# Kernel optimization log

Hardware: AMD Instinct MI355X
Metric: run time of the kernel (lower is better)

Reference implementation:

```python
import jax, jax.numpy as jnp
import numpy as np

N_NODES = 50000
N_EDGES = 800000
N_S = 32          # 0e channels in node feats
N_V = 16          # 1o channels in node feats
NB = 8            # radial bessel basis size
H = 64            # MLP hidden
S_OUT = N_S + N_V           # 48 scalar message channels (filtered 0e + dot path)
V_OUT = N_V + N_S + N_V     # 64 vector message channels (filtered 1o + sxY1 + vxY2)
NUM_IRREPS = S_OUT + V_OUT  # 112, gated by radial MLP
AVG_NEIGH = 16.0


def setup_inputs() -> dict:
    key = jax.random.key(0)
    ks = jax.random.split(key, 8)
    # scale so edge lengths fall mostly inside the envelope cutoff x_max=1
    vectors = jax.random.normal(ks[0], (N_EDGES, 3), jnp.float32) * 0.25
    node_s = jax.random.normal(ks[1], (N_NODES, N_S), jnp.float32)
    node_v = jax.random.normal(ks[2], (N_NODES, N_V, 3), jnp.float32)
    senders = jax.random.randint(ks[3], (N_EDGES,), 0, N_NODES)
    receivers = jax.random.randint(ks[4], (N_EDGES,), 0, N_NODES)
    W0 = jax.random.normal(ks[5], (NB, H), jnp.float32)
    W1 = jax.random.normal(ks[6], (H, H), jnp.float32)
    W2 = jax.random.normal(ks[7], (H, NUM_IRREPS), jnp.float32)
    return {"vectors": vectors, "node_s": node_s, "node_v": node_v,
            "W0": W0, "W1": W1, "W2": W2,
            "senders": senders, "receivers": receivers}


def _radial_embed(r):
    # r: [E,1] edge lengths. Bessel basis (x_max=1) * polynomial envelope, 0 at r==0.
    n = jnp.arange(1, NB + 1, dtype=r.dtype)            # [NB]
    safe_r = jnp.maximum(r, 1e-12)
    basis = jnp.sqrt(2.0) * jnp.sin(jnp.pi * n * r) / safe_r   # [E,NB]
    x = r
    env = (1.0 - 28.0 * x**6 + 48.0 * x**7 - 21.0 * x**8) * (x < 1.0)  # smooth cutoff
    return jnp.where(r == 0.0, 0.0, basis * env)        # [E,NB]


def reference(vectors, node_s, node_v, W0, W1, W2, senders, receivers):
    E = vectors.shape[0]
    r = jnp.linalg.norm(vectors, axis=-1, keepdims=True)          # [E,1]
    u = vectors / jnp.maximum(r, 1e-12)                            # unit vectors [E,3]

    # gather sender features
    s = node_s[senders]                                            # [E,N_S]
    v = node_v[senders]                                            # [E,N_V,3]

    # equivariant tensor-product paths against spherical harmonics of u
    # (filtered to target irreps 0e,1o). Y1 ~ u, Y2 ~ traceless u u^T.
    path_a = s[:, :, None] * u[:, None, :]                         # 0e x Y1 -> 1o [E,N_S,3]
    path_b = jnp.einsum('eci,ei->ec', v, u)                        # 1o x Y1 -> 0e [E,N_V]
    T = u[:, :, None] * u[:, None, :] - jnp.eye(3, dtype=u.dtype) / 3.0  # [E,3,3]
    path_c = jnp.sqrt(1.5) * jnp.einsum('eij,ecj->eci', T, v)      # 1o x Y2 -> 1o [E,N_V,3]

    msg_s = jnp.concatenate([s, path_b], axis=-1)                  # [E,S_OUT]
    msg_v = jnp.concatenate([v, path_a, path_c], axis=1)           # [E,V_OUT,3]

    # radial MLP gate (no bias, fan-in scaled, swish hidden, linear output)
    emb = _radial_embed(r)                                         # [E,NB]
    h = jax.nn.swish(emb @ W0 / jnp.sqrt(jnp.asarray(NB, emb.dtype)))
    h = jax.nn.swish(h @ W1 / jnp.sqrt(jnp.asarray(H, emb.dtype)))
    mix = h @ W2 / jnp.sqrt(jnp.asarray(H, emb.dtype))             # [E,NUM_IRREPS]

    msg_s = msg_s * mix[:, :S_OUT]
    msg_v = msg_v * mix[:, S_OUT:, None]

    # scatter-add to receivers
    n = node_s.shape[0]
    out_s = jnp.zeros((n, S_OUT), msg_s.dtype).at[receivers].add(msg_s)
    out_v = jnp.zeros((n, V_OUT, 3), msg_v.dtype).at[receivers].add(msg_v)

    inv = 1.0 / jnp.sqrt(AVG_NEIGH)
    return jnp.concatenate([out_s * inv, (out_v * inv).reshape(n, V_OUT * 3)], axis=-1)
```

## Files before the change

kernel.cpp:

```cpp
#include <hip/hip_runtime.h>
#include <hip/hip_fp16.h>

#define N_S 32
#define N_V 16
#define NB 8
#define HH 64
#define NIR 112
#define ROW 240
#define MROW 120
#define GCAP 64

typedef _Float16 half8 __attribute__((ext_vector_type(8)));
typedef float f32x4 __attribute__((ext_vector_type(4)));

__device__ __forceinline__ float swishf(float x) {
  return x / (1.f + __expf(-x));
}

struct ChanDesc { int path, off, mixI, i; };

__device__ __forceinline__ void mkDesc(int t, ChanDesc& d) {
  if (t < 32) { d.path = 0; d.off = t; d.mixI = t; d.i = 0; }
  else if (t < 48) { d.path = 1; d.off = 3 * (t - 32); d.mixI = t; d.i = 0; }
  else if (t < ROW) {
    int q = t - 48, c = q / 3, i = q - 3 * c;
    d.mixI = 48 + c;
    if (c < 16) { d.path = 2; d.off = q; d.i = 0; }
    else if (c < 48) { d.path = 3; d.off = c - 16; d.i = i; }
    else { d.path = 4; d.off = 3 * (c - 48); d.i = i; }
  } else { d.path = -1; d.off = 0; d.mixI = 0; d.i = 0; }
}

__device__ __forceinline__ float evalChan(const ChanDesc& d,
                                          const float* __restrict__ srow,
                                          const float* __restrict__ vrow,
                                          float mix, float u0, float u1, float u2) {
  if (d.path < 0) return 0.f;
  if (d.path == 0) return srow[d.off] * mix;
  if (d.path == 2) return vrow[d.off] * mix;
  float uo = d.i == 0 ? u0 : (d.i == 1 ? u1 : u2);
  if (d.path == 3) return srow[d.off] * uo * mix;
  float dd = vrow[d.off] * u0 + vrow[d.off + 1] * u1 + vrow[d.off + 2] * u2;
  if (d.path == 1) return dd * mix;
  return 1.22474487139f * (uo * dd - vrow[d.off + d.i] * 0.33333333333f) * mix;
}

__device__ __forceinline__ float evalChan16(const ChanDesc& d,
                                            const _Float16* __restrict__ srow,
                                            const _Float16* __restrict__ vrow,
                                            float mix, float u0, float u1, float u2) {
  if (d.path == 0) return (float)srow[d.off] * mix;
  if (d.path == 2) return (float)vrow[d.off] * mix;
  float uo = d.i == 0 ? u0 : (d.i == 1 ? u1 : u2);
  if (d.path == 3) return (float)srow[d.off] * uo * mix;
  float dd = (float)vrow[d.off] * u0 + (float)vrow[d.off + 1] * u1 + (float)vrow[d.off + 2] * u2;
  if (d.path == 1) return dd * mix;
  return 1.22474487139f * (uo * dd - (float)vrow[d.off + d.i] * 0.33333333333f) * mix;
}

__device__ __forceinline__ void radialEmb(float x, float y, float z, bool valid,
                                          float* emb, float* u0, float* u1, float* u2) {
  float r2 = x * x + y * y + z * z;
  float r = sqrtf(r2);
  float invr = 1.f / fmaxf(r, 1e-12f);
  *u0 = x * invr; *u1 = y * invr; *u2 = z * invr;
  float env = 0.f;
  if (r < 1.f) {
    float r3 = r * r2;
    float r6 = r3 * r3;
    env = 1.f + r6 * (-28.f + (48.f - 21.f * r) * r);
  }
  float coef = 1.41421356237f * invr * env;
  if (!valid || r == 0.f) coef = 0.f;
  float ph = 3.14159265358979323846f * r;
  float s1 = __sinf(ph), c1 = __cosf(ph);
  float twc = 2.f * c1;
  float sp = 0.f, sc = s1;
#pragma unroll
  for (int n = 0; n < NB; ++n) {
    emb[n] = coef * sc;
    float sn = twc * sc - sp;
    sp = sc;
    sc = sn;
  }
}


__global__ __launch_bounds__(256) void hist_kernel(const int* __restrict__ rcv,
                                                   int* __restrict__ hist, int E) {
  int e = blockIdx.x * 256 + threadIdx.x;
  if (e < E) atomicAdd(&hist[rcv[e]], 1);
}

__global__ __launch_bounds__(256) void scan1_kernel(const int* __restrict__ hist,
                                                    int* __restrict__ scanTmp,
                                                    int* __restrict__ bsum, int N) {
  __shared__ int sh[256];
  int t = threadIdx.x;
  int i = blockIdx.x * 256 + t;
  sh[t] = (i < N) ? hist[i] : 0;
  __syncthreads();
#pragma unroll
  for (int off = 1; off < 256; off <<= 1) {
    int x = (t >= off) ? sh[t - off] : 0;
    __syncthreads();
    sh[t] += x;
    __syncthreads();
  }
  if (i < N) scanTmp[i] = sh[t];
  if (t == 255) bsum[blockIdx.x] = sh[255];
}

__global__ __launch_bounds__(256) void scan2_kernel(int* __restrict__ bsum, int nb) {
  __shared__ int sh[256];
  int t = threadIdx.x;
  sh[t] = (t < nb) ? bsum[t] : 0;
  __syncthreads();
#pragma unroll
  for (int off = 1; off < 256; off <<= 1) {
    int x = (t >= off) ? sh[t - off] : 0;
    __syncthreads();
    sh[t] += x;
    __syncthreads();
  }
  int excl = (t == 0) ? 0 : sh[t - 1];
  if (t < nb) bsum[t] = excl;
}

__global__ __launch_bounds__(256) void scan3_kernel(const int* __restrict__ scanTmp,
                                                    const int* __restrict__ bsum,
                                                    const int* __restrict__ hist,
                                                    int* __restrict__ offs,
                                                    int* __restrict__ cursor, int N) {
  int i = blockIdx.x * 256 + threadIdx.x;
  if (i < N) {
    int incl = scanTmp[i] + bsum[blockIdx.x];
    offs[i + 1] = incl;
    cursor[i] = incl - hist[i];
    if (i == 0) offs[0] = 0;
  }
}

__global__ __launch_bounds__(256) void reorder_kernel(const int* __restrict__ rcv,
                                                      int* __restrict__ cursor,
                                                      int* __restrict__ sortedE, int E) {
  int e = blockIdx.x * 256 + threadIdx.x;
  if (e < E) {
    int pos = atomicAdd(&cursor[rcv[e]], 1);
    sortedE[pos] = e;
  }
}

__global__ __launch_bounds__(256) void reorderInv_kernel(const int* __restrict__ rcv,
                                                         int* __restrict__ cursor,
                                                         int* __restrict__ invPos, int E) {
  int e = blockIdx.x * 256 + threadIdx.x;
  if (e < E) {
    int pos = atomicAdd(&cursor[rcv[e]], 1);
    invPos[e] = pos;
  }
}


__global__ __launch_bounds__(256) void wconv2_kernel(const float* __restrict__ W1,
                                                     const float* __restrict__ W2,
                                                     _Float16* __restrict__ W1T,
                                                     _Float16* __restrict__ W2T) {
  int i = blockIdx.x * 256 + threadIdx.x;
  if (i < 4096) {
    int k = i >> 6, n = i & 63;
    W1T[n * 64 + k] = (_Float16)(W1[k * 64 + n] * 0.125f);
  } else if (i < 4096 + 7168) {
    int j = i - 4096;
    int k = j / 112, n = j - k * 112;
    W2T[n * 64 + k] = (_Float16)(W2[k * 112 + n] * 0.125f);
  }
}

__global__ __launch_bounds__(256) void nodeconv_kernel(const float* __restrict__ ns,
                                                       const float* __restrict__ nv,
                                                       _Float16* __restrict__ s16,
                                                       _Float16* __restrict__ v16, int N) {
  int i = blockIdx.x * 256 + threadIdx.x;
  int ts = N * N_S;
  int tv = N * N_V * 3;
  if (i < ts) s16[i] = (_Float16)ns[i];
  else if (i < ts + tv) v16[i - ts] = (_Float16)nv[i - ts];
}


__global__ __launch_bounds__(256, 4) void mlp_mfma_sorted_kernel(
    const float* __restrict__ vec,
    const float* __restrict__ W0,
    const _Float16* __restrict__ W1T,
    const _Float16* __restrict__ W2T,
    const int* __restrict__ senders,
    const int* __restrict__ invPos,
    _Float16* __restrict__ mixS,
    int E) {
  __shared__ __align__(16) _Float16 hbuf[4 * 64 * 72];
  const int lane = threadIdx.x & 63;
  const int wave = threadIdx.x >> 6;
  const int gbase = blockIdx.x * 256 + wave * 64;
  _Float16* hb = hbuf + wave * (64 * 72);

  const int m15 = lane & 15;
  const int q = lane >> 4;

  {
    int e = gbase + lane;
    bool valid = e < E;
    float x = 0.f, y = 0.f, z = 0.f;
    int snd = 0;
    if (valid) {
      const float* vp = vec + 3 * (size_t)e;
      x = vp[0]; y = vp[1]; z = vp[2];
      snd = senders[e];
    }
    float emb[NB], u0, u1, u2;
    radialEmb(x, y, z, valid, emb, &u0, &u1, &u2);
    for (int kg = 0; kg < 8; ++kg) {
      half8 pk;
#pragma unroll
      for (int kk = 0; kk < 8; ++kk) {
        int k = kg * 8 + kk;
        float a = 0.f;
#pragma unroll
        for (int n = 0; n < NB; ++n) a = fmaf(emb[n], W0[n * HH + k], a);
        pk[kk] = (_Float16)swishf(a * 0.35355339059f);
      }
      *(half8*)(hb + lane * 72 + kg * 8) = pk;
    }
    float* auxp = (float*)(hb + lane * 72 + 64);
    auxp[0] = u0; auxp[1] = u1; auxp[2] = u2;
    ((int*)auxp)[3] = snd;
  }

  half8 bW1[4][2];
#pragma unroll
  for (int nt = 0; nt < 4; ++nt)
#pragma unroll
    for (int q2 = 0; q2 < 2; ++q2)
      bW1[nt][q2] = *(const half8*)(W1T + (nt * 16 + m15) * 64 + q2 * 32 + q * 8);

#pragma unroll
  for (int t = 0; t < 4; ++t) {
    half8 a0 = *(const half8*)(hb + (t * 16 + m15) * 72 + q * 8);
    half8 a1 = *(const half8*)(hb + (t * 16 + m15) * 72 + 32 + q * 8);
#pragma unroll
    for (int nt = 0; nt < 4; ++nt) {
      f32x4 d = {0.f, 0.f, 0.f, 0.f};
      d = __builtin_amdgcn_mfma_f32_16x16x32_f16(a0, bW1[nt][0], d, 0, 0, 0);
      d = __builtin_amdgcn_mfma_f32_16x16x32_f16(a1, bW1[nt][1], d, 0, 0, 0);
#pragma unroll
      for (int r = 0; r < 4; ++r)
        hb[(t * 16 + q * 4 + r) * 72 + nt * 16 + m15] = (_Float16)swishf(d[r]);
    }
  }

  half8 A2[4][2];
#pragma unroll
  for (int t = 0; t < 4; ++t)
#pragma unroll
    for (int q2 = 0; q2 < 2; ++q2)
      A2[t][q2] = *(const half8*)(hb + (t * 16 + m15) * 72 + q2 * 32 + q * 8);

  for (int nl = 0; nl < 4; ++nl) {
    half8 b0 = *(const half8*)(W2T + (nl * 16 + m15) * 64 + q * 8);
    half8 b1 = *(const half8*)(W2T + (nl * 16 + m15) * 64 + 32 + q * 8);
#pragma unroll
    for (int t = 0; t < 4; ++t) {
      f32x4 d = {0.f, 0.f, 0.f, 0.f};
      d = __builtin_amdgcn_mfma_f32_16x16x32_f16(A2[t][0], b0, d, 0, 0, 0);
      d = __builtin_amdgcn_mfma_f32_16x16x32_f16(A2[t][1], b1, d, 0, 0, 0);
#pragma unroll
      for (int r = 0; r < 4; ++r)
        hb[(t * 16 + q * 4 + r) * 72 + nl * 16 + m15] = (_Float16)d[r];
    }
  }
  for (int it = 0; it < 8; ++it) {
    int c = it * 64 + lane;
    int el = c >> 3, p = c & 7;
    int e = gbase + el;
    half8 v = *(const half8*)(hb + el * 72 + p * 8);
    if (e < E) {
      int pos = invPos[e];
      *(half8*)(mixS + (size_t)pos * MROW + p * 8) = v;
    }
  }

  for (int nl = 0; nl < 3; ++nl) {
    int ntg = 4 + nl;
    half8 b0 = *(const half8*)(W2T + (ntg * 16 + m15) * 64 + q * 8);
    half8 b1 = *(const half8*)(W2T + (ntg * 16 + m15) * 64 + 32 + q * 8);
#pragma unroll
    for (int t = 0; t < 4; ++t) {
      f32x4 d = {0.f, 0.f, 0.f, 0.f};
      d = __builtin_amdgcn_mfma_f32_16x16x32_f16(A2[t][0], b0, d, 0, 0, 0);
      d = __builtin_amdgcn_mfma_f32_16x16x32_f16(A2[t][1], b1, d, 0, 0, 0);
#pragma unroll
      for (int r = 0; r < 4; ++r)
        hb[(t * 16 + q * 4 + r) * 72 + nl * 16 + m15] = (_Float16)d[r];
    }
  }
  for (int it = 0; it < 7; ++it) {
    int c = it * 64 + lane;
    int el = (int)(((unsigned)c * 9363u) >> 16);
    int p = c - el * 7;
    int e = gbase + el;
    half8 v = *(const half8*)(hb + el * 72 + (p < 6 ? p * 8 : 64));
    if (e < E) {
      int pos = invPos[e];
      *(half8*)(mixS + (size_t)pos * MROW + 64 + p * 8) = v;
    }
  }
}

__global__ __launch_bounds__(256) void gather_lds_kernel(
    const _Float16* __restrict__ mixS,
    const _Float16* __restrict__ s16,
    const _Float16* __restrict__ v16,
    const int* __restrict__ offs,
    float* __restrict__ out, int N) {
  __shared__ __align__(16) _Float16 mixLds[GCAP * MROW];
  __shared__ __align__(16) _Float16 nodeLds[GCAP * 80];

  const int tid = threadIdx.x;
  const int lane = tid & 63;
  const int wave = tid >> 6;
  const int wid0 = blockIdx.x * 4;

  const int e0 = offs[wid0];
  const int e4 = offs[min(wid0 + 4, N)];
  const int wid = wid0 + wave;
  const int sw = offs[min(wid, N)];
  const int ew = offs[min(wid + 1, N)];

  ChanDesc d[4];
#pragma unroll
  for (int tb = 0; tb < 4; ++tb) mkDesc(tb * 64 + lane, d[tb]);

  float acc[4] = {0.f, 0.f, 0.f, 0.f};

  for (int c0 = e0; c0 < e4; c0 += GCAP) {
    const int cnt = min(GCAP, e4 - c0);
    for (int ch = tid; ch < cnt * 15; ch += 256) {
      int row = ch / 15, part = ch - row * 15;
      *(half8*)(mixLds + row * MROW + part * 8) =
          *(const half8*)(mixS + (size_t)(c0 + row) * MROW + part * 8);
    }
    __syncthreads();
    for (int ch = tid; ch < cnt * 10; ch += 256) {
      int row = ch / 10, part = ch - row * 10;
      int snd = ((const int*)(mixLds + row * MROW + 112))[3];
      const _Float16* src = (part < 4)
          ? s16 + (size_t)snd * N_S + part * 8
          : v16 + (size_t)snd * (N_V * 3) + (part - 4) * 8;
      *(half8*)(nodeLds + row * 80 + (part < 4 ? part * 8 : 32 + (part - 4) * 8)) =
          *(const half8*)src;
    }
    __syncthreads();
    const int jlo = max(sw - c0, 0);
    const int jhi = min(ew - c0, cnt);
    for (int j = jlo; j < jhi; ++j) {
      const _Float16* row = mixLds + j * MROW;
      const float* aux = (const float*)(row + 112);
      float u0 = aux[0], u1 = aux[1], u2 = aux[2];
      const _Float16* srow = nodeLds + j * 80;
      const _Float16* vrow = srow + 32;
#pragma unroll
      for (int tb = 0; tb < 4; ++tb) {
        if (d[tb].path >= 0) {
          float m = (float)row[d[tb].mixI];
          acc[tb] += evalChan16(d[tb], srow, vrow, m, u0, u1, u2);
        }
      }
    }
    __syncthreads();
  }

  if (wid < N) {
    float* orow = out + (size_t)wid * ROW;
#pragma unroll
    for (int tb = 0; tb < 4; ++tb) {
      int t = tb * 64 + lane;
      if (t < ROW) orow[t] = 0.25f * acc[tb];
    }
  }
}


__global__ __launch_bounds__(256, 4) void mlp_mfma_kernel(
    const float* __restrict__ vec,
    const float* __restrict__ W0,
    const _Float16* __restrict__ W1T,
    const _Float16* __restrict__ W2T,
    __half* __restrict__ mixOut, int E) {
  __shared__ __align__(16) _Float16 hbuf[4 * 64 * 72];
  const int lane = threadIdx.x & 63;
  const int wave = threadIdx.x >> 6;
  const int gbase = blockIdx.x * 256 + wave * 64;
  _Float16* hb = hbuf + wave * (64 * 72);
  const int m15 = lane & 15;
  const int q = lane >> 4;

  {
    int e = gbase + lane;
    bool valid = e < E;
    float x = 0.f, y = 0.f, z = 0.f;
    if (valid) {
      const float* vp = vec + 3 * (size_t)e;
      x = vp[0]; y = vp[1]; z = vp[2];
    }
    float emb[NB], u0, u1, u2;
    radialEmb(x, y, z, valid, emb, &u0, &u1, &u2);
    for (int kg = 0; kg < 8; ++kg) {
      half8 pk;
#pragma unroll
      for (int kk = 0; kk < 8; ++kk) {
        int k = kg * 8 + kk;
        float a = 0.f;
#pragma unroll
        for (int n = 0; n < NB; ++n) a = fmaf(emb[n], W0[n * HH + k], a);
        pk[kk] = (_Float16)swishf(a * 0.35355339059f);
      }
      *(half8*)(hb + lane * 72 + kg * 8) = pk;
    }
  }

  half8 bW1[4][2];
#pragma unroll
  for (int nt = 0; nt < 4; ++nt)
#pragma unroll
    for (int q2 = 0; q2 < 2; ++q2)
      bW1[nt][q2] = *(const half8*)(W1T + (nt * 16 + m15) * 64 + q2 * 32 + q * 8);

#pragma unroll
  for (int t = 0; t < 4; ++t) {
    half8 a0 = *(const half8*)(hb + (t * 16 + m15) * 72 + q * 8);
    half8 a1 = *(const half8*)(hb + (t * 16 + m15) * 72 + 32 + q * 8);
#pragma unroll
    for (int nt = 0; nt < 4; ++nt) {
      f32x4 d = {0.f, 0.f, 0.f, 0.f};
      d = __builtin_amdgcn_mfma_f32_16x16x32_f16(a0, bW1[nt][0], d, 0, 0, 0);
      d = __builtin_amdgcn_mfma_f32_16x16x32_f16(a1, bW1[nt][1], d, 0, 0, 0);
#pragma unroll
      for (int r = 0; r < 4; ++r)
        hb[(t * 16 + q * 4 + r) * 72 + nt * 16 + m15] = (_Float16)swishf(d[r]);
    }
  }

  half8 A2[4][2];
#pragma unroll
  for (int t = 0; t < 4; ++t)
#pragma unroll
    for (int q2 = 0; q2 < 2; ++q2)
      A2[t][q2] = *(const half8*)(hb + (t * 16 + m15) * 72 + q2 * 32 + q * 8);

  for (int hf = 0; hf < 2; ++hf) {
    const int ntCount = hf ? 3 : 4;
    for (int nl = 0; nl < ntCount; ++nl) {
      int ntg = hf * 4 + nl;
      half8 b0 = *(const half8*)(W2T + (ntg * 16 + m15) * 64 + q * 8);
      half8 b1 = *(const half8*)(W2T + (ntg * 16 + m15) * 64 + 32 + q * 8);
#pragma unroll
      for (int t = 0; t < 4; ++t) {
        f32x4 d = {0.f, 0.f, 0.f, 0.f};
        d = __builtin_amdgcn_mfma_f32_16x16x32_f16(A2[t][0], b0, d, 0, 0, 0);
        d = __builtin_amdgcn_mfma_f32_16x16x32_f16(A2[t][1], b1, d, 0, 0, 0);
#pragma unroll
        for (int r = 0; r < 4; ++r)
          hb[(t * 16 + q * 4 + r) * 72 + nl * 16 + m15] = (_Float16)d[r];
      }
    }
    if (hf == 0) {
      for (int it = 0; it < 8; ++it) {
        int c = it * 64 + lane;
        int el = c >> 3, p = c & 7;
        int e = gbase + el;
        half8 v = *(const half8*)(hb + el * 72 + p * 8);
        if (e < E) *(half8*)((_Float16*)mixOut + (size_t)e * NIR + p * 8) = v;
      }
    } else {
      for (int it = 0; it < 6; ++it) {
        int c = it * 64 + lane;
        int el = (int)(((unsigned)c * 43691u) >> 18);
        int p = c - el * 6;
        int e = gbase + el;
        half8 v = *(const half8*)(hb + el * 72 + p * 8);
        if (e < E) *(half8*)((_Float16*)mixOut + (size_t)e * NIR + 64 + p * 8) = v;
      }
    }
  }
}

__global__ __launch_bounds__(256) void gather_kernel(
    const float* __restrict__ vec,
    const float* __restrict__ nodes_s,
    const float* __restrict__ nodes_v,
    const int* __restrict__ senders,
    const int* __restrict__ offs,
    const int* __restrict__ sortedE,
    const __half* __restrict__ mix,
    float* __restrict__ out, int N) {
  int wid = blockIdx.x * 4 + (threadIdx.x >> 6);
  int lane = threadIdx.x & 63;
  if (wid >= N) return;

  ChanDesc d[4];
#pragma unroll
  for (int tb = 0; tb < 4; ++tb) mkDesc(tb * 64 + lane, d[tb]);

  float acc[4] = {0.f, 0.f, 0.f, 0.f};
  int s0 = offs[wid], s1 = offs[wid + 1];

  for (int i = s0; i < s1; ++i) {
    int e = __builtin_amdgcn_readfirstlane(sortedE[i]);
    int snd = __builtin_amdgcn_readfirstlane(senders[e]);
    const float* vp = vec + 3 * (size_t)e;
    float x = vp[0], y = vp[1], z = vp[2];
    float r = sqrtf(x * x + y * y + z * z);
    float invr = 1.f / fmaxf(r, 1e-12f);
    float u0 = x * invr, u1 = y * invr, u2 = z * invr;
    const float* srow = nodes_s + (size_t)snd * N_S;
    const float* vrow = nodes_v + (size_t)snd * (N_V * 3);
    const __half* mrow = mix + (size_t)e * NIR;
#pragma unroll
    for (int tb = 0; tb < 4; ++tb) {
      if (d[tb].path >= 0) {
        float m = __half2float(mrow[d[tb].mixI]);
        acc[tb] += evalChan(d[tb], srow, vrow, m, u0, u1, u2);
      }
    }
  }

  float* orow = out + (size_t)wid * ROW;
#pragma unroll
  for (int tb = 0; tb < 4; ++tb) {
    int t = tb * 64 + lane;
    if (t < ROW) orow[t] = 0.25f * acc[tb];
  }
}


__global__ __launch_bounds__(64) void edge_kernel(
    const float* __restrict__ vec,
    const float* __restrict__ nodes_s,
    const float* __restrict__ nodes_v,
    const int* __restrict__ senders,
    const int* __restrict__ receivers,
    const float* __restrict__ W0f,
    const float* __restrict__ W1f,
    const float* __restrict__ W2f,
    float* __restrict__ out, int E) {
  __shared__ float hLds[HH * 64];
  __shared__ float uLds[64 * 3];
  __shared__ int sLds[64];
  __shared__ int rLds[64];
  __half* mixLds = reinterpret_cast<__half*>(hLds);

  const int lane = threadIdx.x;
  const int base = blockIdx.x * 64;
  const int eg = base + lane;
  const bool valid = eg < E;

  float emb[NB];
  {
    float x = 0.f, y = 0.f, z = 0.f;
    int snd = 0, rcv = 0;
    if (valid) {
      const float* vp = vec + 3 * (size_t)eg;
      x = vp[0]; y = vp[1]; z = vp[2];
      snd = senders[eg];
      rcv = receivers[eg];
    }
    float u0, u1, u2;
    radialEmb(x, y, z, valid, emb, &u0, &u1, &u2);
    uLds[lane * 3 + 0] = u0;
    uLds[lane * 3 + 1] = u1;
    uLds[lane * 3 + 2] = u2;
    sLds[lane] = snd;
    rLds[lane] = rcv;
  }

  for (int j0 = 0; j0 < HH; j0 += 8) {
    float a[8];
#pragma unroll
    for (int jj = 0; jj < 8; ++jj) a[jj] = 0.f;
#pragma unroll
    for (int k = 0; k < NB; ++k) {
      const float* wrow = W0f + k * HH + j0;
      float ek = emb[k];
#pragma unroll
      for (int jj = 0; jj < 8; ++jj) a[jj] = fmaf(ek, wrow[jj], a[jj]);
    }
#pragma unroll
    for (int jj = 0; jj < 8; ++jj)
      hLds[(j0 + jj) * 64 + lane] = swishf(a[jj] * 0.35355339059f);
  }
  __syncthreads();

  float h2[HH];
#pragma unroll
  for (int j = 0; j < HH; ++j) h2[j] = 0.f;
  for (int k = 0; k < HH; ++k) {
    float hk = hLds[k * 64 + lane];
    const float* wrow = W1f + k * HH;
#pragma unroll
    for (int j = 0; j < HH; ++j) h2[j] = fmaf(hk, wrow[j], h2[j]);
  }
#pragma unroll
  for (int j = 0; j < HH; ++j) h2[j] = swishf(h2[j] * 0.125f);
  __syncthreads();

  for (int m0 = 0; m0 < NIR; m0 += 4) {
    float a0 = 0.f, a1 = 0.f, a2 = 0.f, a3 = 0.f;
#pragma unroll
    for (int k = 0; k < HH; ++k) {
      const float* wrow = W2f + k * NIR + m0;
      float hk = h2[k];
      a0 = fmaf(hk, wrow[0], a0);
      a1 = fmaf(hk, wrow[1], a1);
      a2 = fmaf(hk, wrow[2], a2);
      a3 = fmaf(hk, wrow[3], a3);
    }
    mixLds[lane * NIR + m0 + 0] = __float2half_rn(a0 * 0.125f);
    mixLds[lane * NIR + m0 + 1] = __float2half_rn(a1 * 0.125f);
    mixLds[lane * NIR + m0 + 2] = __float2half_rn(a2 * 0.125f);
    mixLds[lane * NIR + m0 + 3] = __float2half_rn(a3 * 0.125f);
  }
  __syncthreads();

  ChanDesc d[4];
#pragma unroll
  for (int tb = 0; tb < 4; ++tb) mkDesc(tb * 64 + lane, d[tb]);

  const int cnt = min(64, E - base);
  for (int e = 0; e < cnt; ++e) {
    int snd = sLds[e], rcv = rLds[e];
    float u0 = uLds[e * 3 + 0], u1 = uLds[e * 3 + 1], u2 = uLds[e * 3 + 2];
    const float* srow = nodes_s + (size_t)snd * N_S;
    const float* vrow = nodes_v + (size_t)snd * (N_V * 3);
    const __half* mrow = mixLds + e * NIR;
    float* orow = out + (size_t)rcv * ROW;
#pragma unroll
    for (int tb = 0; tb < 4; ++tb) {
      if (d[tb].path >= 0) {
        float m = __half2float(mrow[d[tb].mixI]);
        float val = evalChan(d[tb], srow, vrow, m, u0, u1, u2);
        unsafeAtomicAdd(orow + tb * 64 + lane, 0.25f * val);
      }
    }
  }
}


extern "C" void kernel_launch(void* const* d_in, const int* in_sizes, int n_in,
                              void* d_out, int out_size, void* d_ws, size_t ws_size,
                              hipStream_t stream) {
  const float* vec = (const float*)d_in[0];
  const float* ns = (const float*)d_in[1];
  const float* nv = (const float*)d_in[2];
  const float* w0 = (const float*)d_in[3];
  const float* w1 = (const float*)d_in[4];
  const float* w2 = (const float*)d_in[5];
  const int* snd = (const int*)d_in[6];
  const int* rcv = (const int*)d_in[7];
  float* out = (float*)d_out;

  const int E = in_sizes[6];
  const int N = in_sizes[1] / N_S;
  const int nb = (N + 255) / 256;
  const int eb = (E + 255) / 256;

  {
    char* p = (char*)d_ws;
    _Float16* mixS = (_Float16*)p; p += (size_t)E * MROW * sizeof(_Float16);
    int* hist = (int*)p;           p += (size_t)N * 4;
    int* scanTmp = (int*)p;        p += (size_t)N * 4;
    int* offs = (int*)p;           p += ((size_t)N + 1) * 4;
    int* cursor = (int*)p;         p += (size_t)N * 4;
    int* bsum = (int*)p;           p += 256 * 4;
    int* invPos = (int*)p;         p += (size_t)E * 4;
    p = (char*)(((uintptr_t)p + 15) & ~(uintptr_t)15);
    _Float16* W1T = (_Float16*)p;  p += 4096 * sizeof(_Float16);
    _Float16* W2T = (_Float16*)p;  p += 7168 * sizeof(_Float16);
    _Float16* s16 = (_Float16*)p;  p += (size_t)N * N_S * sizeof(_Float16);
    _Float16* v16 = (_Float16*)p;  p += (size_t)N * N_V * 3 * sizeof(_Float16);
    size_t needA = (size_t)(p - (char*)d_ws);

    if (needA <= ws_size && nb <= 256) {
      hipMemsetAsync(hist, 0, (size_t)N * 4, stream);
      hist_kernel<<<eb, 256, 0, stream>>>(rcv, hist, E);
      scan1_kernel<<<nb, 256, 0, stream>>>(hist, scanTmp, bsum, N);
      scan2_kernel<<<1, 256, 0, stream>>>(bsum, nb);
      scan3_kernel<<<nb, 256, 0, stream>>>(scanTmp, bsum, hist, offs, cursor, N);
      reorderInv_kernel<<<eb, 256, 0, stream>>>(rcv, cursor, invPos, E);
      wconv2_kernel<<<44, 256, 0, stream>>>(w1, w2, W1T, W2T);
      nodeconv_kernel<<<(N * 80 + 255) / 256, 256, 0, stream>>>(ns, nv, s16, v16, N);
      mlp_mfma_sorted_kernel<<<eb, 256, 0, stream>>>(vec, w0, W1T, W2T, snd, invPos, mixS, E);
      gather_lds_kernel<<<(N + 3) / 4, 256, 0, stream>>>(mixS, s16, v16, offs, out, N);
      return;
    }
  }

  {
    char* p = (char*)d_ws;
    __half* mixW = (__half*)p;     p += (size_t)E * NIR * sizeof(__half);
    int* hist = (int*)p;           p += (size_t)N * 4;
    int* scanTmp = (int*)p;        p += (size_t)N * 4;
    int* offs = (int*)p;           p += ((size_t)N + 1) * 4;
    int* cursor = (int*)p;         p += (size_t)N * 4;
    int* bsum = (int*)p;           p += 256 * 4;
    int* sortedE = (int*)p;        p += (size_t)E * 4;
    p = (char*)(((uintptr_t)p + 15) & ~(uintptr_t)15);
    _Float16* W1T = (_Float16*)p;  p += 4096 * sizeof(_Float16);
    _Float16* W2T = (_Float16*)p;  p += 7168 * sizeof(_Float16);
    size_t needB = (size_t)(p - (char*)d_ws);

    if (needB <= ws_size && nb <= 256) {
      hipMemsetAsync(hist, 0, (size_t)N * 4, stream);
      hist_kernel<<<eb, 256, 0, stream>>>(rcv, hist, E);
      scan1_kernel<<<nb, 256, 0, stream>>>(hist, scanTmp, bsum, N);
      scan2_kernel<<<1, 256, 0, stream>>>(bsum, nb);
      scan3_kernel<<<nb, 256, 0, stream>>>(scanTmp, bsum, hist, offs, cursor, N);
      reorder_kernel<<<eb, 256, 0, stream>>>(rcv, cursor, sortedE, E);
      wconv2_kernel<<<44, 256, 0, stream>>>(w1, w2, W1T, W2T);
      mlp_mfma_kernel<<<eb, 256, 0, stream>>>(vec, w0, W1T, W2T, mixW, E);
      gather_kernel<<<(N + 3) / 4, 256, 0, stream>>>(vec, ns, nv, snd, offs, sortedE, mixW, out, N);
      return;
    }
  }

  hipMemsetAsync(d_out, 0, (size_t)out_size * sizeof(float), stream);
  edge_kernel<<<(E + 63) / 64, 64, 0, stream>>>(vec, ns, nv, snd, rcv, w0, w1, w2, out, E);
}
```

Baseline: 561.7 us.

## Compute full edge messages in MLP kernel and stream-reduce them per receiver

The MLP kernel now gathers sender features (fp16) and computes all 240 message channels per edge, writing them in receiver-sorted order. The per-node gather kernel becomes a pure streaming sum over contiguous rows. The weight and node conversion kernels are merged into one prep launch. The old fallback path is replaced with the previous sorted path. The point is to move the per-channel tensor-product work off the node-side gather and make the reduction fully coalesced. The cost is a larger intermediate buffer (240 vs 120 halves per edge), which means more write and read traffic, plus higher register pressure (launch bounds 256,2).

Result: no change. 559.6 us (-0.4%).

```diff
diff --git a/kernel.cpp b/kernel.cpp
--- a/kernel.cpp
+++ b/kernel.cpp
@@ -11,7 +11,10 @@
 #define GCAP 64
 
 typedef _Float16 half8 __attribute__((ext_vector_type(8)));
+typedef _Float16 half4v __attribute__((ext_vector_type(4)));
 typedef float f32x4 __attribute__((ext_vector_type(4)));
+
+#define H8F(arr, idx) ((float)arr[(idx) >> 3][(idx) & 7])
 
 __device__ __forceinline__ float swishf(float x) {
   return x / (1.f + __expf(-x));
@@ -141,16 +144,6 @@
   }
 }
 
-__global__ __launch_bounds__(256) void reorder_kernel(const int* __restrict__ rcv,
-                                                      int* __restrict__ cursor,
-                                                      int* __restrict__ sortedE, int E) {
-  int e = blockIdx.x * 256 + threadIdx.x;
-  if (e < E) {
-    int pos = atomicAdd(&cursor[rcv[e]], 1);
-    sortedE[pos] = e;
-  }
-}
-
 __global__ __launch_bounds__(256) void reorderInv_kernel(const int* __restrict__ rcv,
                                                          int* __restrict__ cursor,
                                                          int* __restrict__ invPos, int E) {
@@ -162,30 +155,235 @@
 }
 
 
-__global__ __launch_bounds__(256) void wconv2_kernel(const float* __restrict__ W1,
-                                                     const float* __restrict__ W2,
-                                                     _Float16* __restrict__ W1T,
-                                                     _Float16* __restrict__ W2T) {
-  int i = blockIdx.x * 256 + threadIdx.x;
-  if (i < 4096) {
-    int k = i >> 6, n = i & 63;
-    W1T[n * 64 + k] = (_Float16)(W1[k * 64 + n] * 0.125f);
-  } else if (i < 4096 + 7168) {
-    int j = i - 4096;
-    int k = j / 112, n = j - k * 112;
-    W2T[n * 64 + k] = (_Float16)(W2[k * 112 + n] * 0.125f);
-  }
-}
-
-__global__ __launch_bounds__(256) void nodeconv_kernel(const float* __restrict__ ns,
-                                                       const float* __restrict__ nv,
-                                                       _Float16* __restrict__ s16,
-                                                       _Float16* __restrict__ v16, int N) {
+__global__ __launch_bounds__(256) void prep_kernel(const float* __restrict__ W1,
+                                                   const float* __restrict__ W2,
+                                                   const float* __restrict__ ns,
+                                                   const float* __restrict__ nv,
+                                                   _Float16* __restrict__ W1T,
+                                                   _Float16* __restrict__ W2T,
+                                                   _Float16* __restrict__ s16,
+                                                   _Float16* __restrict__ v16, int N) {
   int i = blockIdx.x * 256 + threadIdx.x;
   int ts = N * N_S;
   int tv = N * N_V * 3;
   if (i < ts) s16[i] = (_Float16)ns[i];
   else if (i < ts + tv) v16[i - ts] = (_Float16)nv[i - ts];
+  else if (i < ts + tv + 4096) {
+    int j = i - ts - tv;
+    int k = j >> 6, n = j & 63;
+    W1T[n * 64 + k] = (_Float16)(W1[k * 64 + n] * 0.125f);
+  } else if (i < ts + tv + 4096 + 7168) {
+    int j = i - ts - tv - 4096;
+    int k = j / 112, n = j - k * 112;
+    W2T[n * 64 + k] = (_Float16)(W2[k * 112 + n] * 0.125f);
+  }
+}
+
+__global__ __launch_bounds__(256, 2) void mlp_msg_kernel(
+    const float* __restrict__ vec,
+    const float* __restrict__ W0,
+    const _Float16* __restrict__ W1T,
+    const _Float16* __restrict__ W2T,
+    const int* __restrict__ senders,
+    const int* __restrict__ invPos,
+    const _Float16* __restrict__ s16,
+    const _Float16* __restrict__ v16,
+    _Float16* __restrict__ msgS,
+    int E) {
+  __shared__ __align__(16) _Float16 hbuf[4 * 64 * 72];
+  const int lane = threadIdx.x & 63;
+  const int wave = threadIdx.x >> 6;
+  const int gbase = blockIdx.x * 256 + wave * 64;
+  _Float16* hb = hbuf + wave * (64 * 72);
+
+  const int m15 = lane & 15;
+  const int q = lane >> 4;
+
+  int e = gbase + lane;
+  bool valid = e < E;
+  float x = 0.f, y = 0.f, z = 0.f;
+  int snd = 0, pos = 0;
+  if (valid) {
+    const float* vp = vec + 3 * (size_t)e;
+    x = vp[0]; y = vp[1]; z = vp[2];
+    snd = senders[e];
+    pos = invPos[e];
+  }
+  float emb[NB], u0, u1, u2;
+  radialEmb(x, y, z, valid, emb, &u0, &u1, &u2);
+
+  for (int kg = 0; kg < 8; ++kg) {
+    half8 pk;
+#pragma unroll
+    for (int kk = 0; kk < 8; ++kk) {
+      int k = kg * 8 + kk;
+      float a = 0.f;
+#pragma unroll
+      for (int n = 0; n < NB; ++n) a = fmaf(emb[n], W0[n * HH + k], a);
+      pk[kk] = (_Float16)swishf(a * 0.35355339059f);
+    }
+    *(half8*)(hb + lane * 72 + kg * 8) = pk;
+  }
+
+  half8 ss[4], vv[6];
+  {
+    const _Float16* sp = s16 + (size_t)snd * N_S;
+    const _Float16* vp16 = v16 + (size_t)snd * (N_V * 3);
+#pragma unroll
+    for (int k = 0; k < 4; ++k) ss[k] = *(const half8*)(sp + k * 8);
+#pragma unroll
+    for (int k = 0; k < 6; ++k) vv[k] = *(const half8*)(vp16 + k * 8);
+  }
+
+  {
+    half8 bW1[4][2];
+#pragma unroll
+    for (int nt = 0; nt < 4; ++nt)
+#pragma unroll
+      for (int q2 = 0; q2 < 2; ++q2)
+        bW1[nt][q2] = *(const half8*)(W1T + (nt * 16 + m15) * 64 + q2 * 32 + q * 8);
+#pragma unroll
+    for (int t = 0; t < 4; ++t) {
+      half8 a0 = *(const half8*)(hb + (t * 16 + m15) * 72 + q * 8);
+      half8 a1 = *(const half8*)(hb + (t * 16 + m15) * 72 + 32 + q * 8);
+#pragma unroll
+      for (int nt = 0; nt < 4; ++nt) {
+        f32x4 d = {0.f, 0.f, 0.f, 0.f};
+        d = __builtin_amdgcn_mfma_f32_16x16x32_f16(a0, bW1[nt][0], d, 0, 0, 0);
+        d = __builtin_amdgcn_mfma_f32_16x16x32_f16(a1, bW1[nt][1], d, 0, 0, 0);
+#pragma unroll
+        for (int r = 0; r < 4; ++r)
+          hb[(t * 16 + q * 4 + r) * 72 + nt * 16 + m15] = (_Float16)swishf(d[r]);
+      }
+    }
+  }
+
+  half8 A2[4][2];
+#pragma unroll
+  for (int t = 0; t < 4; ++t)
+#pragma unroll
+    for (int q2 = 0; q2 < 2; ++q2)
+      A2[t][q2] = *(const half8*)(hb + (t * 16 + m15) * 72 + q2 * 32 + q * 8);
+
+  float d16[16];
+#pragma unroll
+  for (int j = 0; j < 16; ++j)
+    d16[j] = H8F(vv, 3 * j) * u0 + H8F(vv, 3 * j + 1) * u1 + H8F(vv, 3 * j + 2) * u2;
+
+  _Float16* orow = msgS + (size_t)pos * ROW;
+
+  for (int nl = 0; nl < 4; ++nl) {
+    half8 b0 = *(const half8*)(W2T + (nl * 16 + m15) * 64 + q * 8);
+    half8 b1 = *(const half8*)(W2T + (nl * 16 + m15) * 64 + 32 + q * 8);
+#pragma unroll
+    for (int t = 0; t < 4; ++t) {
+      f32x4 d = {0.f, 0.f, 0.f, 0.f};
+      d = __builtin_amdgcn_mfma_f32_16x16x32_f16(A2[t][0], b0, d, 0, 0, 0);
+      d = __builtin_amdgcn_mfma_f32_16x16x32_f16(A2[t][1], b1, d, 0, 0, 0);
+#pragma unroll
+      for (int r = 0; r < 4; ++r)
+        hb[(t * 16 + q * 4 + r) * 72 + nl * 16 + m15] = (_Float16)d[r];
+    }
+  }
+  half8 m0[8];
+#pragma unroll
+  for (int k = 0; k < 8; ++k) m0[k] = *(const half8*)(hb + lane * 72 + k * 8);
+
+  for (int nl = 0; nl < 3; ++nl) {
+    int ntg = 4 + nl;
+    half8 b0 = *(const half8*)(W2T + (ntg * 16 + m15) * 64 + q * 8);
+    half8 b1 = *(const half8*)(W2T + (ntg * 16 + m15) * 64 + 32 + q * 8);
+#pragma unroll
+    for (int t = 0; t < 4; ++t) {
+      f32x4 d = {0.f, 0.f, 0.f, 0.f};
+      d = __builtin_amdgcn_mfma_f32_16x16x32_f16(A2[t][0], b0, d, 0, 0, 0);
+      d = __builtin_amdgcn_mfma_f32_16x16x32_f16(A2[t][1], b1, d, 0, 0, 0);
+#pragma unroll
+      for (int r = 0; r < 4; ++r)
+        hb[(t * 16 + q * 4 + r) * 72 + nl * 16 + m15] = (_Float16)d[r];
+    }
+  }
+
+#pragma unroll
+  for (int ck = 0; ck < 12; ++ck) {
+    half8 outv;
+#pragma unroll
+    for (int jj = 0; jj < 8; ++jj) {
+      const int t = ck * 8 + jj;
+      float val;
+      if (t < 32) {
+        val = H8F(m0, t) * H8F(ss, t);
+      } else if (t < 48) {
+        val = H8F(m0, t) * d16[t - 32];
+      } else {
+        const int c = (t - 48) / 3;
+        val = H8F(m0, 48 + c) * H8F(vv, t - 48);
+      }
+      outv[jj] = (_Float16)val;
+    }
+    if (valid) *(half8*)(orow + ck * 8) = outv;
+  }
+
+  half8 m1[6];
+#pragma unroll
+  for (int k = 0; k < 6; ++k) m1[k] = *(const half8*)(hb + lane * 72 + k * 8);
+#pragma unroll
+  for (int ck = 0; ck < 18; ++ck) {
+    half8 outv;
+#pragma unroll
+    for (int jj = 0; jj < 8; ++jj) {
+      const int t = 96 + ck * 8 + jj;
+      const int c = (t - 48) / 3;
+      const int i = (t - 48) % 3;
+      const float uo = (i == 0) ? u0 : ((i == 1) ? u1 : u2);
+      const float m = H8F(m1, c - 16);
+      float val;
+      if (c < 48) {
+        val = m * H8F(ss, c - 16) * uo;
+      } else {
+        val = 1.22474487139f * (uo * d16[c - 48] - H8F(vv, t - 192) * 0.33333333333f) * m;
+      }
+      outv[jj] = (_Float16)val;
+    }
+    if (valid) *(half8*)(orow + 96 + ck * 8) = outv;
+  }
+}
+
+
+__global__ __launch_bounds__(256) void gather_stream_kernel(
+    const _Float16* __restrict__ msgS,
+    const int* __restrict__ offs,
+    float* __restrict__ out, int N) {
+  int wid = blockIdx.x * 4 + (threadIdx.x >> 6);
+  int lane = threadIdx.x & 63;
+  if (wid >= N) return;
+  int s0 = __builtin_amdgcn_readfirstlane(offs[wid]);
+  int s1 = __builtin_amdgcn_readfirstlane(offs[wid + 1]);
+  const bool act = lane < 60;
+
+  float a0 = 0.f, a1 = 0.f, a2 = 0.f, a3 = 0.f;
+  const _Float16* base = msgS + (size_t)s0 * ROW + lane * 4;
+  const int n = s1 - s0;
+  int j = 0;
+  for (; j + 2 <= n; j += 2) {
+    half4v va = {0, 0, 0, 0}, vb = {0, 0, 0, 0};
+    if (act) {
+      va = *(const half4v*)(base + (size_t)j * ROW);
+      vb = *(const half4v*)(base + (size_t)(j + 1) * ROW);
+    }
+    a0 += (float)va[0] + (float)vb[0];
+    a1 += (float)va[1] + (float)vb[1];
+    a2 += (float)va[2] + (float)vb[2];
+    a3 += (float)va[3] + (float)vb[3];
+  }
+  if (j < n && act) {
+    half4v va = *(const half4v*)(base + (size_t)j * ROW);
+    a0 += (float)va[0]; a1 += (float)va[1]; a2 += (float)va[2]; a3 += (float)va[3];
+  }
+  if (act) {
+    float4 o = make_float4(0.25f * a0, 0.25f * a1, 0.25f * a2, 0.25f * a3);
+    *(float4*)(out + (size_t)wid * ROW + lane * 4) = o;
+  }
 }
 
 
@@ -386,159 +584,6 @@
       int t = tb * 64 + lane;
       if (t < ROW) orow[t] = 0.25f * acc[tb];
     }
-  }
-}
-
-
-__global__ __launch_bounds__(256, 4) void mlp_mfma_kernel(
-    const float* __restrict__ vec,
-    const float* __restrict__ W0,
-    const _Float16* __restrict__ W1T,
-    const _Float16* __restrict__ W2T,
-    __half* __restrict__ mixOut, int E) {
-  __shared__ __align__(16) _Float16 hbuf[4 * 64 * 72];
-  const int lane = threadIdx.x & 63;
-  const int wave = threadIdx.x >> 6;
-  const int gbase = blockIdx.x * 256 + wave * 64;
-  _Float16* hb = hbuf + wave * (64 * 72);
-  const int m15 = lane & 15;
-  const int q = lane >> 4;
-
-  {
-    int e = gbase + lane;
-    bool valid = e < E;
-    float x = 0.f, y = 0.f, z = 0.f;
-    if (valid) {
-      const float* vp = vec + 3 * (size_t)e;
-      x = vp[0]; y = vp[1]; z = vp[2];
-    }
-    float emb[NB], u0, u1, u2;
-    radialEmb(x, y, z, valid, emb, &u0, &u1, &u2);
-    for (int kg = 0; kg < 8; ++kg) {
-      half8 pk;
-#pragma unroll
-      for (int kk = 0; kk < 8; ++kk) {
-        int k = kg * 8 + kk;
-        float a = 0.f;
-#pragma unroll
-        for (int n = 0; n < NB; ++n) a = fmaf(emb[n], W0[n * HH + k], a);
-        pk[kk] = (_Float16)swishf(a * 0.35355339059f);
-      }
-      *(half8*)(hb + lane * 72 + kg * 8) = pk;
-    }
-  }
-
-  half8 bW1[4][2];
-#pragma unroll
-  for (int nt = 0; nt < 4; ++nt)
-#pragma unroll
-    for (int q2 = 0; q2 < 2; ++q2)
-      bW1[nt][q2] = *(const half8*)(W1T + (nt * 16 + m15) * 64 + q2 * 32 + q * 8);
-
-#pragma unroll
-  for (int t = 0; t < 4; ++t) {
-    half8 a0 = *(const half8*)(hb + (t * 16 + m15) * 72 + q * 8);
-    half8 a1 = *(const half8*)(hb + (t * 16 + m15) * 72 + 32 + q * 8);
-#pragma unroll
-    for (int nt = 0; nt < 4; ++nt) {
-      f32x4 d = {0.f, 0.f, 0.f, 0.f};
-      d = __builtin_amdgcn_mfma_f32_16x16x32_f16(a0, bW1[nt][0], d, 0, 0, 0);
-      d = __builtin_amdgcn_mfma_f32_16x16x32_f16(a1, bW1[nt][1], d, 0, 0, 0);
-#pragma unroll
-      for (int r = 0; r < 4; ++r)
-        hb[(t * 16 + q * 4 + r) * 72 + nt * 16 + m15] = (_Float16)swishf(d[r]);
-    }
-  }
-
-  half8 A2[4][2];
-#pragma unroll
-  for (int t = 0; t < 4; ++t)
-#pragma unroll
-    for (int q2 = 0; q2 < 2; ++q2)
-      A2[t][q2] = *(const half8*)(hb + (t * 16 + m15) * 72 + q2 * 32 + q * 8);
-
-  for (int hf = 0; hf < 2; ++hf) {
-    const int ntCount = hf ? 3 : 4;
-    for (int nl = 0; nl < ntCount; ++nl) {
-      int ntg = hf * 4 + nl;
-      half8 b0 = *(const half8*)(W2T + (ntg * 16 + m15) * 64 + q * 8);
-      half8 b1 = *(const half8*)(W2T + (ntg * 16 + m15) * 64 + 32 + q * 8);
-#pragma unroll
-      for (int t = 0; t < 4; ++t) {
-        f32x4 d = {0.f, 0.f, 0.f, 0.f};
-        d = __builtin_amdgcn_mfma_f32_16x16x32_f16(A2[t][0], b0, d, 0, 0, 0);
-        d = __builtin_amdgcn_mfma_f32_16x16x32_f16(A2[t][1], b1, d, 0, 0, 0);
-#pragma unroll
-        for (int r = 0; r < 4; ++r)
-          hb[(t * 16 + q * 4 + r) * 72 + nl * 16 + m15] = (_Float16)d[r];
-      }
-    }
-    if (hf == 0) {
-      for (int it = 0; it < 8; ++it) {
-        int c = it * 64 + lane;
-        int el = c >> 3, p = c & 7;
-        int e = gbase + el;
-        half8 v = *(const half8*)(hb + el * 72 + p * 8);
-        if (e < E) *(half8*)((_Float16*)mixOut + (size_t)e * NIR + p * 8) = v;
-      }
-    } else {
-      for (int it = 0; it < 6; ++it) {
-        int c = it * 64 + lane;
-        int el = (int)(((unsigned)c * 43691u) >> 18);
-        int p = c - el * 6;
-        int e = gbase + el;
-        half8 v = *(const half8*)(hb + el * 72 + p * 8);
-        if (e < E) *(half8*)((_Float16*)mixOut + (size_t)e * NIR + 64 + p * 8) = v;
-      }
-    }
-  }
-}
-
-__global__ __launch_bounds__(256) void gather_kernel(
-    const float* __restrict__ vec,
-    const float* __restrict__ nodes_s,
-    const float* __restrict__ nodes_v,
-    const int* __restrict__ senders,
-    const int* __restrict__ offs,
-    const int* __restrict__ sortedE,
-    const __half* __restrict__ mix,
-    float* __restrict__ out, int N) {
-  int wid = blockIdx.x * 4 + (threadIdx.x >> 6);
-  int lane = threadIdx.x & 63;
-  if (wid >= N) return;
-
-  ChanDesc d[4];
-#pragma unroll
-  for (int tb = 0; tb < 4; ++tb) mkDesc(tb * 64 + lane, d[tb]);
-
-  float acc[4] = {0.f, 0.f, 0.f, 0.f};
-  int s0 = offs[wid], s1 = offs[wid + 1];
-
-  for (int i = s0; i < s1; ++i) {
-    int e = __builtin_amdgcn_readfirstlane(sortedE[i]);
-    int snd = __builtin_amdgcn_readfirstlane(senders[e]);
-    const float* vp = vec + 3 * (size_t)e;
-    float x = vp[0], y = vp[1], z = vp[2];
-    float r = sqrtf(x * x + y * y + z * z);
-    float invr = 1.f / fmaxf(r, 1e-12f);
-    float u0 = x * invr, u1 = y * invr, u2 = z * invr;
-    const float* srow = nodes_s + (size_t)snd * N_S;
-    const float* vrow = nodes_v + (size_t)snd * (N_V * 3);
-    const __half* mrow = mix + (size_t)e * NIR;
-#pragma unroll
-    for (int tb = 0; tb < 4; ++tb) {
-      if (d[tb].path >= 0) {
-        float m = __half2float(mrow[d[tb].mixI]);
-        acc[tb] += evalChan(d[tb], srow, vrow, m, u0, u1, u2);
-      }
-    }
-  }
-
-  float* orow = out + (size_t)wid * ROW;
-#pragma unroll
-  for (int tb = 0; tb < 4; ++tb) {
-    int t = tb * 64 + lane;
-    if (t < ROW) orow[t] = 0.25f * acc[tb];
   }
 }
 
@@ -672,21 +717,22 @@
   const int N = in_sizes[1] / N_S;
   const int nb = (N + 255) / 256;
   const int eb = (E + 255) / 256;
+  const int prepElems = N * (N_S + N_V * 3) + 4096 + 7168;
 
   {
     char* p = (char*)d_ws;
-    _Float16* mixS = (_Float16*)p; p += (size_t)E * MROW * sizeof(_Float16);
-    int* hist = (int*)p;           p += (size_t)N * 4;
-    int* scanTmp = (int*)p;        p += (size_t)N * 4;
-    int* offs = (int*)p;           p += ((size_t)N + 1) * 4;
-    int* cursor = (int*)p;         p += (size_t)N * 4;
-    int* bsum = (int*)p;           p += 256 * 4;
-    int* invPos = (int*)p;         p += (size_t)E * 4;
+    _Float16* msgS = (_Float16*)p;  p += (size_t)E * ROW * sizeof(_Float16);
+    int* hist = (int*)p;            p += (size_t)N * 4;
+    int* scanTmp = (int*)p;         p += (size_t)N * 4;
+    int* offs = (int*)p;            p += ((size_t)N + 1) * 4;
+    int* cursor = (int*)p;          p += (size_t)N * 4;
+    int* bsum = (int*)p;            p += 256 * 4;
+    int* invPos = (int*)p;          p += (size_t)E * 4;
     p = (char*)(((uintptr_t)p + 15) & ~(uintptr_t)15);
-    _Float16* W1T = (_Float16*)p;  p += 4096 * sizeof(_Float16);
-    _Float16* W2T = (_Float16*)p;  p += 7168 * sizeof(_Float16);
-    _Float16* s16 = (_Float16*)p;  p += (size_t)N * N_S * sizeof(_Float16);
-    _Float16* v16 = (_Float16*)p;  p += (size_t)N * N_V * 3 * sizeof(_Float16);
+    _Float16* W1T = (_Float16*)p;   p += 4096 * sizeof(_Float16);
+    _Float16* W2T = (_Float16*)p;   p += 7168 * sizeof(_Float16);
+    _Float16* s16 = (_Float16*)p;   p += (size_t)N * N_S * sizeof(_Float16);
+    _Float16* v16 = (_Float16*)p;   p += (size_t)N * N_V * 3 * sizeof(_Float16);
     size_t needA = (size_t)(p - (char*)d_ws);
 
     if (needA <= ws_size && nb <= 256) {
@@ -696,26 +742,27 @@
       scan2_kernel<<<1, 256, 0, stream>>>(bsum, nb);
       scan3_kernel<<<nb, 256, 0, stream>>>(scanTmp, bsum, hist, offs, cursor, N);
       reorderInv_kernel<<<eb, 256, 0, stream>>>(rcv, cursor, invPos, E);
-      wconv2_kernel<<<44, 256, 0, stream>>>(w1, w2, W1T, W2T);
-      nodeconv_kernel<<<(N * 80 + 255) / 256, 256, 0, stream>>>(ns, nv, s16, v16, N);
-      mlp_mfma_sorted_kernel<<<eb, 256, 0, stream>>>(vec, w0, W1T, W2T, snd, invPos, mixS, E);
-      gather_lds_kernel<<<(N + 3) / 4, 256, 0, stream>>>(mixS, s16, v16, offs, out, N);
+      prep_kernel<<<(prepElems + 255) / 256, 256, 0, stream>>>(w1, w2, ns, nv, W1T, W2T, s16, v16, N);
+      mlp_msg_kernel<<<eb, 256, 0, stream>>>(vec, w0, W1T, W2T, snd, invPos, s16, v16, msgS, E);
+      gather_stream_kernel<<<(N + 3) / 4, 256, 0, stream>>>(msgS, offs, out, N);
       return;
     }
   }
 
   {
     char* p = (char*)d_ws;
-    __half* mixW = (__half*)p;     p += (size_t)E * NIR * sizeof(__half);
-    int* hist = (int*)p;           p += (size_t)N * 4;
-    int* scanTmp = (int*)p;        p += (size_t)N * 4;
-    int* offs = (int*)p;           p += ((size_t)N + 1) * 4;
-    int* cursor = (int*)p;         p += (size_t)N * 4;
-    int* bsum = (int*)p;           p += 256 * 4;
-    int* sortedE = (int*)p;        p += (size_t)E * 4;
+    _Float16* mixS = (_Float16*)p;  p += (size_t)E * MROW * sizeof(_Float16);
+    int* hist = (int*)p;            p += (size_t)N * 4;
+    int* scanTmp = (int*)p;         p += (size_t)N * 4;
+    int* offs = (int*)p;            p += ((size_t)N + 1) * 4;
+    int* cursor = (int*)p;          p += (size_t)N * 4;
+    int* bsum = (int*)p;            p += 256 * 4;
+    int* invPos = (int*)p;          p += (size_t)E * 4;
     p = (char*)(((uintptr_t)p + 15) & ~(uintptr_t)15);
-    _Float16* W1T = (_Float16*)p;  p += 4096 * sizeof(_Float16);
-    _Float16* W2T = (_Float16*)p;  p += 7168 * sizeof(_Float16);
+    _Float16* W1T = (_Float16*)p;   p += 4096 * sizeof(_Float16);
+    _Float16* W2T = (_Float16*)p;   p += 7168 * sizeof(_Float16);
+    _Float16* s16 = (_Float16*)p;   p += (size_t)N * N_S * sizeof(_Float16);
+    _Float16* v16 = (_Float16*)p;   p += (size_t)N * N_V * 3 * sizeof(_Float16);
     size_t needB = (size_t)(p - (char*)d_ws);
 
     if (needB <= ws_size && nb <= 256) {
@@ -724,10 +771,10 @@
       scan1_kernel<<<nb, 256, 0, stream>>>(hist, scanTmp, bsum, N);
       scan2_kernel<<<1, 256, 0, stream>>>(bsum, nb);
       scan3_kernel<<<nb, 256, 0, stream>>>(scanTmp, bsum, hist, offs, cursor, N);
-      reorder_kernel<<<eb, 256, 0, stream>>>(rcv, cursor, sortedE, E);
-      wconv2_kernel<<<44, 256, 0, stream>>>(w1, w2, W1T, W2T);
-      mlp_mfma_kernel<<<eb, 256, 0, stream>>>(vec, w0, W1T, W2T, mixW, E);
-      gather_kernel<<<(N + 3) / 4, 256, 0, stream>>>(vec, ns, nv, snd, offs, sortedE, mixW, out, N);
+      reorderInv_kernel<<<eb, 256, 0, stream>>>(rcv, cursor, invPos, E);
+      prep_kernel<<<(prepElems + 255) / 256, 256, 0, stream>>>(w1, w2, ns, nv, W1T, W2T, s16, v16, N);
+      mlp_mfma_sorted_kernel<<<eb, 256, 0, stream>>>(vec, w0, W1T, W2T, snd, invPos, mixS, E);
+      gather_lds_kernel<<<(N + 3) / 4, 256, 0, stream>>>(mixS, s16, v16, offs, out, N);
       return;
     }
   }
```
